# Kernel tuning notes

Hardware: AMD Instinct MI355X
Metric: run time of the kernel (lower is better)

## Reference

```python
import jax, jax.numpy as jnp
import numpy as np

BETA = 0.25  # commitment_beta


def setup_inputs() -> dict:
    key = jax.random.key(0)
    k1, k2 = jax.random.split(key)
    x = jax.random.normal(k1, (8, 256, 32, 32), dtype=jnp.float32)
    # nn.Embedding weight, uniform(-1/K, 1/K) in the original; use small randn-scaled init
    K, d = 4096, 256
    embed_w = jax.random.uniform(k2, (K, d), dtype=jnp.float32, minval=-1.0 / K, maxval=1.0 / K)
    return {"x": x, "embed_w": embed_w}


def reference(x, embed_w):
    B, C, H, W = x.shape
    N = H * W
    # b c h w -> b (h w) c
    xr = jnp.transpose(x, (0, 2, 3, 1)).reshape(B, N, C)
    flat = xr.reshape(B * N, C)
    dist = (-jnp.sum(flat * flat, axis=1, keepdims=True)
            - jnp.sum(embed_w * embed_w, axis=1)
            + 2.0 * jnp.einsum('nd,kd->nk', flat, embed_w))
    # temp=0.0 -> gumbel_sample degenerates to argmax
    embed_ind = jnp.argmax(dist, axis=-1).reshape(B, N)
    x_q = embed_w[embed_ind]  # [B, N, C] gather
    sg = jax.lax.stop_gradient
    loss = (BETA * jnp.mean((sg(x_q) - xr) ** 2)
            + jnp.mean((x_q - sg(xr)) ** 2))
    # straight-through estimator
    x_q = xr + sg(x_q - xr)
    # b (h w) c -> b c h w
    x_q = jnp.transpose(x_q.reshape(B, H, W, C), (0, 3, 1, 2))
    embed_ind = embed_ind.reshape(B, H, W)
    return (x_q, loss, embed_ind)
```

## Files before the change

kernel.cpp:

```cpp
#include <hip/hip_runtime.h>
#include <stdint.h>


typedef _Float16 f16;
typedef f16 half8 __attribute__((ext_vector_type(8)));
typedef float f32x4 __attribute__((ext_vector_type(4)));

__device__ __forceinline__ unsigned int sortable_f32(float v) {
    unsigned int u = __float_as_uint(v);
    return (u & 0x80000000u) ? ~u : (u | 0x80000000u);
}

__device__ __forceinline__ void gload_lds16(const void* g, void* l) {
    __builtin_amdgcn_global_load_lds(
        (const __attribute__((address_space(1))) unsigned int*)g,
        (__attribute__((address_space(3))) unsigned int*)l, 16, 0, 0);
}

__global__ void vq_prep(const float* __restrict__ x, const float* __restrict__ ew,
                        float* __restrict__ e2, float* __restrict__ negx2,
                        unsigned long long* __restrict__ cand,
                        f16* __restrict__ ehi, f16* __restrict__ elo,
                        f16* __restrict__ xhi, f16* __restrict__ xlo,
                        float* __restrict__ loss_cell) {
    __shared__ float xs[32][132];
    const int u = blockIdx.x, tid = threadIdx.x;
    if (u < 512) {
        const int t = u * 256 + tid;
        const int k = t >> 5, g32 = t & 31;
        const float4 v0 = *(const float4*)(ew + k * 256 + g32 * 8);
        const float4 v1 = *(const float4*)(ew + k * 256 + g32 * 8 + 4);
        const float vf[8] = {v0.x, v0.y, v0.z, v0.w, v1.x, v1.y, v1.z, v1.w};
        half8 h1, h2;
#pragma unroll
        for (int j = 0; j < 8; ++j) {
            const float v = vf[j] * 4096.0f;
            const f16 a = (f16)v;
            const f16 b = (f16)(v - (float)a);
            h1[j] = a; h2[j] = b;
        }
        const int kt = k >> 7, kk = k & 127, ci = g32 >> 2, g = g32 & 3;
        const long off = ((long)((kt * 8 + ci) * 128 + kk)) * 32 + ((g ^ (kk & 3)) * 8);
        *(half8*)(ehi + off) = h1;
        *(half8*)(elo + off) = h2;
    } else if (u < 544) {
        if (tid < 128) {
            const int k = (u - 512) * 128 + tid;
            const float4* row = (const float4*)(ew + k * 256);
            float s = 0.0f;
#pragma unroll 8
            for (int i = 0; i < 64; ++i) {
                float4 v = row[i];
                s += v.x * v.x + v.y * v.y + v.z * v.z + v.w * v.w;
            }
            e2[k] = s;
        }
    } else if (u < 576) {
        const int z = (u - 544) * 256 + tid;
        cand[z] = 0ull;
        if (z == 0) *loss_cell = 0.0f;
    } else if (u < 640) {
        if (tid < 128) {
            const int r = (u - 576) * 128 + tid;
            const int b = r >> 10, n = r & 1023;
            const float* px = x + b * 262144 + n;
            float s = 0.0f;
#pragma unroll 16
            for (int c = 0; c < 256; ++c) {
                float v = px[c << 10];
                s += v * v;
            }
            negx2[r] = -s;
        }
    } else {
        const int unit = u - 640;
        const int ci = unit & 7, mt = unit >> 3;
        const int b = mt >> 3, n0 = (mt & 7) * 128, c0 = ci * 32;
#pragma unroll
        for (int it = 0; it < 4; ++it) {
            const int idx = tid + it * 256;
            const int cc = idx >> 5, nn4 = idx & 31;
            float4 v = *(const float4*)(x + b * 262144 + (c0 + cc) * 1024 + n0 + nn4 * 4);
            *(float4*)&xs[cc][nn4 * 4] = v;
        }
        __syncthreads();
#pragma unroll
        for (int it = 0; it < 2; ++it) {
            const int idx = tid + it * 256;
            const int mm = idx & 127, g = idx >> 7;
            half8 h1, h2;
#pragma unroll
            for (int j = 0; j < 8; ++j) {
                const float v = xs[g * 8 + j][mm];
                const f16 a = (f16)v;
                const f16 bb = (f16)(v - (float)a);
                h1[j] = a; h2[j] = bb;
            }
            const long off = ((long)((mt * 8 + ci) * 128 + mm)) * 32 + ((g ^ (mm & 3)) * 8);
            *(half8*)(xhi + off) = h1;
            *(half8*)(xlo + off) = h2;
        }
    }
}

__launch_bounds__(256, 2)
__global__ void vq_gemm(const f16* __restrict__ xhi, const f16* __restrict__ xlo,
                        const f16* __restrict__ ehi, const f16* __restrict__ elo,
                        const float* __restrict__ e2, const float* __restrict__ negx2,
                        unsigned long long* __restrict__ cand) {
    __shared__ __align__(16) f16 lds[8192];
    const int tid = threadIdx.x;
    const int kt = blockIdx.x, mt = blockIdx.y;
    const int lane = tid & 63, wave = tid >> 6;
    const int wm = wave >> 1, wk = wave & 1;
    const int col = lane & 15, quad = lane >> 4;

    f32x4 acc[4][4] = {};

    const f16* gx[2] = { xhi + (size_t)(mt * 8) * 4096, xlo + (size_t)(mt * 8) * 4096 };
    const f16* geh = ehi + (size_t)(kt * 8) * 4096;
    const f16* gel = elo + (size_t)(kt * 8) * 4096;

    int aoff[4], boff[4];
#pragma unroll
    for (int i = 0; i < 4; ++i) {
        const int m = wm * 64 + i * 16 + col;
        aoff[i] = m * 32 + ((quad ^ (m & 3)) * 8);
        const int k = wk * 64 + i * 16 + col;
        boff[i] = k * 32 + ((quad ^ (k & 3)) * 8);
    }

    for (int ci = 0; ci < 8; ++ci) {
        __syncthreads();
        const int go = ci * 4096 + tid * 8;
        char* lb = (char*)lds + wave * 1024;
#pragma unroll
        for (int p = 0; p < 2; ++p) {
            gload_lds16(gx[p] + go,        lb + p * 8192);
            gload_lds16(gx[p] + go + 2048, lb + p * 8192 + 4096);
        }
        half8 bhi4[4], blo4[4];
#pragma unroll
        for (int j = 0; j < 4; ++j) {
            bhi4[j] = *(const half8*)(geh + ci * 4096 + boff[j]);
            blo4[j] = *(const half8*)(gel + ci * 4096 + boff[j]);
        }
        __syncthreads();

        half8 ahi4[4], alo4[4];
#pragma unroll
        for (int i = 0; i < 4; ++i) {
            ahi4[i] = *(const half8*)&lds[aoff[i]];
            alo4[i] = *(const half8*)&lds[4096 + aoff[i]];
        }
#pragma unroll
        for (int i = 0; i < 4; ++i)
#pragma unroll
            for (int j = 0; j < 4; ++j) {
                acc[i][j] = __builtin_amdgcn_mfma_f32_16x16x32_f16(ahi4[i], bhi4[j], acc[i][j], 0, 0, 0);
                acc[i][j] = __builtin_amdgcn_mfma_f32_16x16x32_f16(ahi4[i], blo4[j], acc[i][j], 0, 0, 0);
                acc[i][j] = __builtin_amdgcn_mfma_f32_16x16x32_f16(alo4[i], bhi4[j], acc[i][j], 0, 0, 0);
            }
    }

    const int m0 = mt * 128 + wm * 64, k0 = kt * 128 + wk * 64;
#pragma unroll
    for (int i = 0; i < 4; ++i)
#pragma unroll
        for (int r = 0; r < 4; ++r) {
            const float A = negx2[m0 + i * 16 + quad * 4 + r];
            unsigned long long bk = 0ull;
#pragma unroll
            for (int j = 0; j < 4; ++j) {
                const int k = k0 + j * 16 + col;
                const float t1 = A - e2[k];
                const float dist = t1 + acc[i][j][r] * 0x1p-11f;
                const unsigned long long key =
                    ((unsigned long long)sortable_f32(dist) << 32)
                    | (unsigned long long)(unsigned int)(4095 - k);
                if (key > bk) bk = key;
            }
#pragma unroll
            for (int mask = 1; mask <= 8; mask <<= 1) {
                const unsigned long long o = __shfl_xor(bk, mask, 64);
                if (o > bk) bk = o;
            }
            if (col == i * 4 + r)
                atomicMax(&cand[m0 + i * 16 + quad * 4 + r], bk);
        }
}

__global__ void vq_out(const float* __restrict__ ew,
                       const unsigned long long* __restrict__ cand,
                       float* __restrict__ out) {
    __shared__ int sidx[64];
    const int tid = threadIdx.x;
    const int r0 = blockIdx.x * 64;
    const int cq0 = blockIdx.y * 64;
    const int b = r0 >> 10, n0 = r0 & 1023;

    if (tid < 64) {
        const int r = r0 + tid;
        const unsigned long long bk = cand[r];
        const int idx = 4095 - (int)(unsigned int)(bk & 0xFFFFFFFFull);
        sidx[tid] = idx;
        if (cq0 == 0) {
            out[2097153 + r] = (float)idx;
            const unsigned int s = (unsigned int)(bk >> 32);
            const unsigned int ubits = (s & 0x80000000u) ? (s & 0x7FFFFFFFu) : ~s;
            float nd = -__uint_as_float(ubits);
#pragma unroll
            for (int m = 1; m <= 32; m <<= 1) nd += __shfl_xor(nd, m, 64);
            if (tid == 0)
                atomicAdd(&out[2097152], 1.25f * (nd / 2097152.0f));
        }
    }
    __syncthreads();

    const int nn = tid & 63, cq = tid >> 6;
    const float* erow = ew + (size_t)sidx[nn] * 256 + cq0;
    float* ocol = out + (size_t)b * 262144 + ((size_t)cq0 << 10) + n0 + nn;
#pragma unroll
    for (int cb = 0; cb < 16; ++cb) {
        const int c = cb * 4 + cq;
        ocol[(size_t)c << 10] = erow[c];
    }
}

extern "C" void kernel_launch(void* const* d_in, const int* in_sizes, int n_in,
                              void* d_out, int out_size, void* d_ws, size_t ws_size,
                              hipStream_t stream) {
    const float* x  = (const float*)d_in[0];
    const float* ew = (const float*)d_in[1];
    float* out = (float*)d_out;

    float* e2 = (float*)d_ws;
    float* negx2 = e2 + 4096;
    unsigned long long* cand = (unsigned long long*)((char*)d_ws + 49152);
    f16* ehi = (f16*)((char*)d_ws + 114688);
    f16* elo = (f16*)((char*)d_ws + 114688 + 2097152);
    f16* xhi = (f16*)out;
    f16* xlo = (f16*)(out + 1048576);

    vq_prep<<<1152, 256, 0, stream>>>(x, ew, e2, negx2, cand,
                                      ehi, elo, xhi, xlo, out + 2097152);
    vq_gemm<<<dim3(32, 64), 256, 0, stream>>>(xhi, xlo, ehi, elo, e2, negx2, cand);
    vq_out<<<dim3(128, 4), 256, 0, stream>>>(ew, cand, out);
}
```

Baseline: 147.7 us.

## Double GEMM M-tile to 256 rows per block and split output gather finer

```diff
diff --git a/kernel.cpp b/kernel.cpp
--- a/kernel.cpp
+++ b/kernel.cpp
@@ -108,37 +108,44 @@
                         const f16* __restrict__ ehi, const f16* __restrict__ elo,
                         const float* __restrict__ e2, const float* __restrict__ negx2,
                         unsigned long long* __restrict__ cand) {
-    __shared__ __align__(16) f16 lds[8192];
+    __shared__ __align__(16) f16 lds[16384];
     const int tid = threadIdx.x;
-    const int kt = blockIdx.x, mt = blockIdx.y;
+    const int kt = blockIdx.x, mtb = blockIdx.y;
     const int lane = tid & 63, wave = tid >> 6;
     const int wm = wave >> 1, wk = wave & 1;
     const int col = lane & 15, quad = lane >> 4;
 
-    f32x4 acc[4][4] = {};
-
-    const f16* gx[2] = { xhi + (size_t)(mt * 8) * 4096, xlo + (size_t)(mt * 8) * 4096 };
+    f32x4 acc[8][4] = {};
+
+    const f16* gxh = xhi + (size_t)(mtb * 16) * 4096;
+    const f16* gxl = xlo + (size_t)(mtb * 16) * 4096;
     const f16* geh = ehi + (size_t)(kt * 8) * 4096;
     const f16* gel = elo + (size_t)(kt * 8) * 4096;
 
-    int aoff[4], boff[4];
-#pragma unroll
-    for (int i = 0; i < 4; ++i) {
-        const int m = wm * 64 + i * 16 + col;
-        aoff[i] = m * 32 + ((quad ^ (m & 3)) * 8);
-        const int k = wk * 64 + i * 16 + col;
-        boff[i] = k * 32 + ((quad ^ (k & 3)) * 8);
+    int aoff[8], boff[4];
+#pragma unroll
+    for (int i = 0; i < 8; ++i) {
+        const int lr = i * 16 + col;
+        aoff[i] = wm * 4096 + lr * 32 + ((quad ^ (lr & 3)) * 8);
+    }
+#pragma unroll
+    for (int j = 0; j < 4; ++j) {
+        const int k = wk * 64 + j * 16 + col;
+        boff[j] = k * 32 + ((quad ^ (k & 3)) * 8);
     }
 
     for (int ci = 0; ci < 8; ++ci) {
         __syncthreads();
         const int go = ci * 4096 + tid * 8;
         char* lb = (char*)lds + wave * 1024;
-#pragma unroll
-        for (int p = 0; p < 2; ++p) {
-            gload_lds16(gx[p] + go,        lb + p * 8192);
-            gload_lds16(gx[p] + go + 2048, lb + p * 8192 + 4096);
-        }
+        gload_lds16(gxh + go,                 lb);
+        gload_lds16(gxh + go + 2048,          lb + 4096);
+        gload_lds16(gxh + go + 32768,         lb + 8192);
+        gload_lds16(gxh + go + 32768 + 2048,  lb + 12288);
+        gload_lds16(gxl + go,                 lb + 16384);
+        gload_lds16(gxl + go + 2048,          lb + 20480);
+        gload_lds16(gxl + go + 32768,         lb + 24576);
+        gload_lds16(gxl + go + 32768 + 2048,  lb + 28672);
         half8 bhi4[4], blo4[4];
 #pragma unroll
         for (int j = 0; j < 4; ++j) {
@@ -147,25 +154,22 @@
         }
         __syncthreads();
 
-        half8 ahi4[4], alo4[4];
-#pragma unroll
-        for (int i = 0; i < 4; ++i) {
-            ahi4[i] = *(const half8*)&lds[aoff[i]];
-            alo4[i] = *(const half8*)&lds[4096 + aoff[i]];
-        }
-#pragma unroll
-        for (int i = 0; i < 4; ++i)
+#pragma unroll
+        for (int i = 0; i < 8; ++i) {
+            const half8 ah = *(const half8*)&lds[aoff[i]];
+            const half8 al = *(const half8*)&lds[8192 + aoff[i]];
 #pragma unroll
             for (int j = 0; j < 4; ++j) {
-                acc[i][j] = __builtin_amdgcn_mfma_f32_16x16x32_f16(ahi4[i], bhi4[j], acc[i][j], 0, 0, 0);
-                acc[i][j] = __builtin_amdgcn_mfma_f32_16x16x32_f16(ahi4[i], blo4[j], acc[i][j], 0, 0, 0);
-                acc[i][j] = __builtin_amdgcn_mfma_f32_16x16x32_f16(alo4[i], bhi4[j], acc[i][j], 0, 0, 0);
-            }
-    }
-
-    const int m0 = mt * 128 + wm * 64, k0 = kt * 128 + wk * 64;
-#pragma unroll
-    for (int i = 0; i < 4; ++i)
+                acc[i][j] = __builtin_amdgcn_mfma_f32_16x16x32_f16(ah, bhi4[j], acc[i][j], 0, 0, 0);
+                acc[i][j] = __builtin_amdgcn_mfma_f32_16x16x32_f16(ah, blo4[j], acc[i][j], 0, 0, 0);
+                acc[i][j] = __builtin_amdgcn_mfma_f32_16x16x32_f16(al, bhi4[j], acc[i][j], 0, 0, 0);
+            }
+        }
+    }
+
+    const int m0 = mtb * 256 + wm * 128, k0 = kt * 128 + wk * 64;
+#pragma unroll
+    for (int i = 0; i < 8; ++i)
 #pragma unroll
         for (int r = 0; r < 4; ++r) {
             const float A = negx2[m0 + i * 16 + quad * 4 + r];
@@ -185,7 +189,7 @@
                 const unsigned long long o = __shfl_xor(bk, mask, 64);
                 if (o > bk) bk = o;
             }
-            if (col == i * 4 + r)
+            if (col == ((i * 4 + r) & 15))
                 atomicMax(&cand[m0 + i * 16 + quad * 4 + r], bk);
         }
 }
@@ -196,7 +200,7 @@
     __shared__ int sidx[64];
     const int tid = threadIdx.x;
     const int r0 = blockIdx.x * 64;
-    const int cq0 = blockIdx.y * 64;
+    const int cq0 = blockIdx.y * 32;
     const int b = r0 >> 10, n0 = r0 & 1023;
 
     if (tid < 64) {
@@ -204,7 +208,7 @@
         const unsigned long long bk = cand[r];
         const int idx = 4095 - (int)(unsigned int)(bk & 0xFFFFFFFFull);
         sidx[tid] = idx;
-        if (cq0 == 0) {
+        if (blockIdx.y == 0) {
             out[2097153 + r] = (float)idx;
             const unsigned int s = (unsigned int)(bk >> 32);
             const unsigned int ubits = (s & 0x80000000u) ? (s & 0x7FFFFFFFu) : ~s;
@@ -221,7 +225,7 @@
     const float* erow = ew + (size_t)sidx[nn] * 256 + cq0;
     float* ocol = out + (size_t)b * 262144 + ((size_t)cq0 << 10) + n0 + nn;
 #pragma unroll
-    for (int cb = 0; cb < 16; ++cb) {
+    for (int cb = 0; cb < 8; ++cb) {
         const int c = cb * 4 + cq;
         ocol[(size_t)c << 10] = erow[c];
     }
@@ -244,6 +248,6 @@
 
     vq_prep<<<1152, 256, 0, stream>>>(x, ew, e2, negx2, cand,
                                       ehi, elo, xhi, xlo, out + 2097152);
-    vq_gemm<<<dim3(32, 64), 256, 0, stream>>>(xhi, xlo, ehi, elo, e2, negx2, cand);
-    vq_out<<<dim3(128, 4), 256, 0, stream>>>(ew, cand, out);
-}
+    vq_gemm<<<dim3(32, 32), 256, 0, stream>>>(xhi, xlo, ehi, elo, e2, negx2, cand);
+    vq_out<<<dim3(128, 8), 256, 0, stream>>>(ew, cand, out);
+}
```

After: 164.1 us. +11.1%, slower.
